# Kernel tuning notes

Hardware: AMD Instinct MI355X
Metric: run time of the kernel (lower is better)

## Reference

```python
import jax, jax.numpy as jnp
import numpy as np

N = 100000
IN_C = 256
OUT_C = 128
NHEAD = 4
NUM_CLASSES = 1000


def setup_inputs() -> dict:
    key = jax.random.key(0)
    ks = jax.random.split(key, 6)
    context_h = jax.random.normal(ks[0], (N, IN_C), dtype=jnp.float32)
    W_lin = jax.random.normal(ks[1], (NHEAD * OUT_C, IN_C), dtype=jnp.float32) * 0.05
    b_lin = jax.random.normal(ks[2], (NHEAD * OUT_C,), dtype=jnp.float32) * 0.05
    W_att = jax.random.normal(ks[3], (OUT_C,), dtype=jnp.float32) * 0.05
    b_att = jax.random.normal(ks[4], (1,), dtype=jnp.float32) * 0.05
    context_y = jax.random.randint(ks[5], (N,), 0, NUM_CLASSES, dtype=jnp.int32)
    return {
        "context_h": context_h,
        "W_lin": W_lin,
        "b_lin": b_lin,
        "W_att": W_att,
        "b_att": b_att,
        "context_y": context_y,
        "num_classes": NUM_CLASSES,
    }


def reference(context_h, W_lin, b_lin, W_att, b_att, context_y, num_classes):
    # Linear projection: [N, nhead*out_c] -> [N, nhead, out_c]
    h = context_h @ W_lin.T + b_lin
    n = context_h.shape[0]
    ht = h.reshape(n, NHEAD, OUT_C)
    # per-head attention score: [N, nhead]
    score = jnp.einsum("nho,o->nh", ht, W_att) + b_att[0]
    score = jnp.where(score >= 0, score, 0.2 * score)  # leaky_relu(0.2)
    # scatter softmax over segments context_y (stable two-pass)
    seg_max = jax.ops.segment_max(score, context_y, num_segments=num_classes)
    p = jnp.exp(score - seg_max[context_y])  # [N, nhead]
    denom = jax.ops.segment_sum(p, context_y, num_segments=num_classes)
    att_w = p / denom[context_y]  # [N, nhead]
    # weighted scatter-add pooling: [N, nhead, in_c] -> [C, nhead, in_c]
    att_h = context_h[:, None, :] * att_w[:, :, None]
    pooled = jax.ops.segment_sum(att_h, context_y, num_segments=num_classes)
    return pooled.reshape(num_classes, NHEAD * IN_C)
```

## Files before the change

### kernel.cpp

```cpp
#include <hip/hip_runtime.h>
#include <math.h>

#define N_ROWS 100000
#define IN_C   256
#define OUT_C  128
#define NHEAD  4
#define NCLS   1000
#define NCOPY  16
#define CAP    64

#define OFF_V      0
#define OFF_CB     1024
#define OFF_CNT    1032
#define OFF_BUCKET 17032

__global__ __launch_bounds__(256) void k_prep(const float* __restrict__ W_lin,
                                              const float* __restrict__ b_lin,
                                              const float* __restrict__ W_att,
                                              const float* __restrict__ b_att,
                                              float* __restrict__ ws) {
    const int b = blockIdx.x, t = threadIdx.x;
    if (b >= NHEAD) {
        int i = (b - NHEAD) * 256 + t;
        if (i < NCOPY * NCLS) ((unsigned*)(ws + OFF_CNT))[i] = 0u;
        return;
    }
    __shared__ float sw[OUT_C];
    __shared__ float rb[256];
    if (t < OUT_C) sw[t] = W_att[t];
    __syncthreads();
    const float* wl = W_lin + (size_t)(b * OUT_C) * IN_C + t;
    float s0 = 0.f, s1 = 0.f, s2 = 0.f, s3 = 0.f;
    #pragma unroll 8
    for (int o = 0; o < OUT_C; o += 4) {
        s0 = fmaf(wl[(size_t)(o + 0) * IN_C], sw[o + 0], s0);
        s1 = fmaf(wl[(size_t)(o + 1) * IN_C], sw[o + 1], s1);
        s2 = fmaf(wl[(size_t)(o + 2) * IN_C], sw[o + 2], s2);
        s3 = fmaf(wl[(size_t)(o + 3) * IN_C], sw[o + 3], s3);
    }
    (ws + OFF_V)[b * IN_C + t] = (s0 + s1) + (s2 + s3);
    rb[t] = (t < OUT_C) ? b_lin[b * OUT_C + t] * sw[t] : 0.f;
    __syncthreads();
    for (int d = 128; d; d >>= 1) {
        if (t < d) rb[t] += rb[t + d];
        __syncthreads();
    }
    if (t == 0) (ws + OFF_CB)[b] = rb[0] + b_att[0];
}

__global__ __launch_bounds__(256) void k_bucket(const int* __restrict__ y,
                                                float* __restrict__ ws) {
    int n = blockIdx.x * 256 + threadIdx.x;
    if (n >= N_ROWS) return;
    unsigned* cnt    = (unsigned*)(ws + OFF_CNT);
    unsigned* bucket = (unsigned*)(ws + OFF_BUCKET);
    unsigned idx = (blockIdx.x & (NCOPY - 1)) * NCLS + (unsigned)y[n];
    unsigned pos = atomicAdd(&cnt[idx], 1u);
    if (pos < CAP) bucket[idx * CAP + pos] = (unsigned)n;
}

__global__ __launch_bounds__(512) void k_pool(const float* __restrict__ ch,
                                              float* __restrict__ out,
                                              const float* __restrict__ ws) {
    __shared__ unsigned rowbuf[NCOPY * CAP];
    __shared__ float4   sAcc[NHEAD][4][64];
    __shared__ float4   sDs[8];
    const int c = blockIdx.x, t = threadIdx.x;
    const int wave = t >> 6, lane = t & 63;
    const unsigned* cntA   = (const unsigned*)(ws + OFF_CNT);
    const unsigned* bucket = (const unsigned*)(ws + OFF_BUCKET);
    float* o = out + (size_t)c * (NHEAD * IN_C);

    unsigned cc[NCOPY], pre[NCOPY];
    unsigned cnt = 0;
    #pragma unroll
    for (int cp = 0; cp < NCOPY; ++cp) {
        unsigned v = cntA[cp * NCLS + c];
        cc[cp] = v > CAP ? CAP : v;
        pre[cp] = cnt;
        cnt += cc[cp];
    }
    if (cnt == 0) {
        if (t < 256) ((float4*)o)[t] = make_float4(0.f, 0.f, 0.f, 0.f);
        return;
    }
    for (int tt = t; tt < NCOPY * CAP; tt += 512) {
        int cp = tt >> 6, j = tt & (CAP - 1);
        if ((unsigned)j < cc[cp])
            rowbuf[pre[cp] + j] = bucket[(cp * NCLS + c) * CAP + j];
    }
    __syncthreads();

    const float4* V4 = (const float4*)(ws + OFF_V);
    float4 v0 = V4[0 * 64 + lane];
    float4 v1 = V4[1 * 64 + lane];
    float4 v2 = V4[2 * 64 + lane];
    float4 v3 = V4[3 * 64 + lane];
    float4 cbv = *(const float4*)(ws + OFF_CB);
    float cb = (lane & 1) ? ((lane & 2) ? cbv.w : cbv.y)
                          : ((lane & 2) ? cbv.z : cbv.x);

    const float4* ch4 = (const float4*)ch;
    const float4 z = make_float4(0.f, 0.f, 0.f, 0.f);

    float4 a0 = z, a1 = z, a2 = z, a3 = z, dsum = z;
    {
        unsigned r = 2 * (unsigned)wave;
        float4 xA0 = z, xA1 = z, xB0 = z, xB1 = z;
        if (r < cnt)      xA0 = ch4[(size_t)rowbuf[r] * 64 + lane];
        if (r + 1 < cnt)  xA1 = ch4[(size_t)rowbuf[r + 1] * 64 + lane];
        if (r + 16 < cnt) xB0 = ch4[(size_t)rowbuf[r + 16] * 64 + lane];
        if (r + 17 < cnt) xB1 = ch4[(size_t)rowbuf[r + 17] * 64 + lane];
        for (; r < cnt; r += 16) {
            unsigned rc = r + 32;
            float4 xC0 = z, xC1 = z;
            if (rc < cnt)     xC0 = ch4[(size_t)rowbuf[rc] * 64 + lane];
            if (rc + 1 < cnt) xC1 = ch4[(size_t)rowbuf[rc + 1] * 64 + lane];

            #pragma unroll
            for (int k = 0; k < 2; ++k) {
                const float4 x = k ? xA1 : xA0;
                const float g = k ? ((r + 1 < cnt) ? 1.f : 0.f) : 1.f;
                float p0 = x.x * v0.x + x.y * v0.y + x.z * v0.z + x.w * v0.w;
                float p1 = x.x * v1.x + x.y * v1.y + x.z * v1.z + x.w * v1.w;
                float p2 = x.x * v2.x + x.y * v2.y + x.z * v2.z + x.w * v2.w;
                float p3 = x.x * v3.x + x.y * v3.y + x.z * v3.z + x.w * v3.w;
                float a01 = (lane & 1) ? p1 : p0;
                float b01 = (lane & 1) ? p0 : p1;
                b01 = __shfl_xor(b01, 1);  a01 += b01;
                float a23 = (lane & 1) ? p3 : p2;
                float b23 = (lane & 1) ? p2 : p3;
                b23 = __shfl_xor(b23, 1);  a23 += b23;
                float e = (lane & 2) ? a23 : a01;
                float f = (lane & 2) ? a01 : a23;
                f = __shfl_xor(f, 2);      e += f;
                e += __shfl_xor(e, 4);
                e += __shfl_xor(e, 8);
                e += __shfl_xor(e, 16);
                e += __shfl_xor(e, 32);
                float s = e + cb;
                s = s >= 0.0f ? s : 0.2f * s;
                float pe = expf(s) * g;
                float h0 = __shfl(pe, 0), h1 = __shfl(pe, 1);
                float h2 = __shfl(pe, 2), h3 = __shfl(pe, 3);
                dsum.x += h0; dsum.y += h1; dsum.z += h2; dsum.w += h3;
                a0.x = fmaf(x.x, h0, a0.x); a0.y = fmaf(x.y, h0, a0.y);
                a0.z = fmaf(x.z, h0, a0.z); a0.w = fmaf(x.w, h0, a0.w);
                a1.x = fmaf(x.x, h1, a1.x); a1.y = fmaf(x.y, h1, a1.y);
                a1.z = fmaf(x.z, h1, a1.z); a1.w = fmaf(x.w, h1, a1.w);
                a2.x = fmaf(x.x, h2, a2.x); a2.y = fmaf(x.y, h2, a2.y);
                a2.z = fmaf(x.z, h2, a2.z); a2.w = fmaf(x.w, h2, a2.w);
                a3.x = fmaf(x.x, h3, a3.x); a3.y = fmaf(x.y, h3, a3.y);
                a3.z = fmaf(x.z, h3, a3.z); a3.w = fmaf(x.w, h3, a3.w);
            }
            xA0 = xB0; xA1 = xB1; xB0 = xC0; xB1 = xC1;
        }
    }
    if (wave < 4) {
        sAcc[0][wave][lane] = a0; sAcc[1][wave][lane] = a1;
        sAcc[2][wave][lane] = a2; sAcc[3][wave][lane] = a3;
    }
    if (lane == 0) sDs[wave] = dsum;
    __syncthreads();
    if (wave >= 4) {
        int w = wave - 4;
        float4 q;
        q = sAcc[0][w][lane]; q.x += a0.x; q.y += a0.y; q.z += a0.z; q.w += a0.w; sAcc[0][w][lane] = q;
        q = sAcc[1][w][lane]; q.x += a1.x; q.y += a1.y; q.z += a1.z; q.w += a1.w; sAcc[1][w][lane] = q;
        q = sAcc[2][w][lane]; q.x += a2.x; q.y += a2.y; q.z += a2.z; q.w += a2.w; sAcc[2][w][lane] = q;
        q = sAcc[3][w][lane]; q.x += a3.x; q.y += a3.y; q.z += a3.z; q.w += a3.w; sAcc[3][w][lane] = q;
    }
    __syncthreads();

    if (wave < NHEAD) {
        float4 q0 = sAcc[wave][0][lane], q1 = sAcc[wave][1][lane],
               q2 = sAcc[wave][2][lane], q3 = sAcc[wave][3][lane];
        float4 acc = make_float4((q0.x + q1.x) + (q2.x + q3.x),
                                 (q0.y + q1.y) + (q2.y + q3.y),
                                 (q0.z + q1.z) + (q2.z + q3.z),
                                 (q0.w + q1.w) + (q2.w + q3.w));
        float4 d0 = sDs[0], d1 = sDs[1], d2 = sDs[2], d3 = sDs[3];
        float4 d4 = sDs[4], d5 = sDs[5], d6 = sDs[6], d7 = sDs[7];
        float4 dt = make_float4(((d0.x + d1.x) + (d2.x + d3.x)) + ((d4.x + d5.x) + (d6.x + d7.x)),
                                ((d0.y + d1.y) + (d2.y + d3.y)) + ((d4.y + d5.y) + (d6.y + d7.y)),
                                ((d0.z + d1.z) + (d2.z + d3.z)) + ((d4.z + d5.z) + (d6.z + d7.z)),
                                ((d0.w + d1.w) + (d2.w + d3.w)) + ((d4.w + d5.w) + (d6.w + d7.w)));
        float dh = (wave == 0) ? dt.x : (wave == 1) ? dt.y : (wave == 2) ? dt.z : dt.w;
        float inv = 1.0f / dh;
        ((float4*)o)[wave * 64 + lane] =
            make_float4(acc.x * inv, acc.y * inv, acc.z * inv, acc.w * inv);
    }
}

extern "C" void kernel_launch(void* const* d_in, const int* in_sizes, int n_in,
                              void* d_out, int out_size, void* d_ws, size_t ws_size,
                              hipStream_t stream) {
    const float* ch    = (const float*)d_in[0];
    const float* W_lin = (const float*)d_in[1];
    const float* b_lin = (const float*)d_in[2];
    const float* W_att = (const float*)d_in[3];
    const float* b_att = (const float*)d_in[4];
    const int*   y     = (const int*)d_in[5];
    float* out = (float*)d_out;
    float* ws  = (float*)d_ws;

    k_prep  <<<NHEAD + 63, 256, 0, stream>>>(W_lin, b_lin, W_att, b_att, ws);
    k_bucket<<<(N_ROWS + 255) / 256, 256, 0, stream>>>(y, ws);
    k_pool  <<<NCLS, 512, 0, stream>>>(ch, out, ws);
}
```

Before: 184.7 us.

## Split per-class pooling across four blocks and merge partials in a separate kernel

The pooling kernel used to run one 512-thread block per class, so only 1000 large blocks covered the GPU. It now launches four 256-thread blocks per class, each covering a quarter of the bucket copies and writing partial weighted sums and denominators to workspace. A new merge kernel adds the partials and normalises. This aims for better load balance and occupancy, at the cost of an extra launch and extra global traffic for the partials (about 16 MB written and then read back).

```diff
diff --git a/kernel.cpp b/kernel.cpp
--- a/kernel.cpp
+++ b/kernel.cpp
@@ -8,11 +8,15 @@
 #define NCLS   1000
 #define NCOPY  16
 #define CAP    64
+#define SPLIT  4
+#define CPS    (NCOPY / SPLIT)
 
 #define OFF_V      0
 #define OFF_CB     1024
 #define OFF_CNT    1032
 #define OFF_BUCKET 17032
+#define OFF_PART   1041032
+#define OFF_PDEN   5137032
 
 __global__ __launch_bounds__(256) void k_prep(const float* __restrict__ W_lin,
                                               const float* __restrict__ b_lin,
@@ -59,35 +63,38 @@
     if (pos < CAP) bucket[idx * CAP + pos] = (unsigned)n;
 }
 
-__global__ __launch_bounds__(512) void k_pool(const float* __restrict__ ch,
-                                              float* __restrict__ out,
-                                              const float* __restrict__ ws) {
-    __shared__ unsigned rowbuf[NCOPY * CAP];
-    __shared__ float4   sAcc[NHEAD][4][64];
-    __shared__ float4   sDs[8];
-    const int c = blockIdx.x, t = threadIdx.x;
-    const int wave = t >> 6, lane = t & 63;
+__global__ __launch_bounds__(256) void k_pool_part(const float* __restrict__ ch,
+                                                   float* __restrict__ ws) {
+    __shared__ unsigned rowbuf[CPS * CAP];
+    __shared__ float4   sAcc[NHEAD][2][64];
+    __shared__ float4   sDs[4];
+    const int c = blockIdx.x >> 2, seg = blockIdx.x & (SPLIT - 1);
+    const int t = threadIdx.x, wave = t >> 6, lane = t & 63;
     const unsigned* cntA   = (const unsigned*)(ws + OFF_CNT);
     const unsigned* bucket = (const unsigned*)(ws + OFF_BUCKET);
-    float* o = out + (size_t)c * (NHEAD * IN_C);
-
-    unsigned cc[NCOPY], pre[NCOPY];
+    float* part = ws + OFF_PART + (size_t)(seg * NCLS + c) * 1024;
+    float* pden = ws + OFF_PDEN + (seg * NCLS + c) * 4;
+    const float4 z = make_float4(0.f, 0.f, 0.f, 0.f);
+
+    unsigned cc[CPS], pre[CPS];
     unsigned cnt = 0;
     #pragma unroll
-    for (int cp = 0; cp < NCOPY; ++cp) {
-        unsigned v = cntA[cp * NCLS + c];
-        cc[cp] = v > CAP ? CAP : v;
-        pre[cp] = cnt;
-        cnt += cc[cp];
+    for (int j = 0; j < CPS; ++j) {
+        unsigned v = cntA[(seg * CPS + j) * NCLS + c];
+        cc[j] = v > CAP ? CAP : v;
+        pre[j] = cnt;
+        cnt += cc[j];
     }
     if (cnt == 0) {
-        if (t < 256) ((float4*)o)[t] = make_float4(0.f, 0.f, 0.f, 0.f);
+        ((float4*)part)[t] = z;
+        if (t < 4) pden[t] = 0.f;
         return;
     }
-    for (int tt = t; tt < NCOPY * CAP; tt += 512) {
-        int cp = tt >> 6, j = tt & (CAP - 1);
-        if ((unsigned)j < cc[cp])
-            rowbuf[pre[cp] + j] = bucket[(cp * NCLS + c) * CAP + j];
+    if (t < CAP) {
+        #pragma unroll
+        for (int j = 0; j < CPS; ++j)
+            if ((unsigned)t < cc[j])
+                rowbuf[pre[j] + t] = bucket[((seg * CPS + j) * NCLS + c) * CAP + t];
     }
     __syncthreads();
 
@@ -101,18 +108,17 @@
                           : ((lane & 2) ? cbv.z : cbv.x);
 
     const float4* ch4 = (const float4*)ch;
-    const float4 z = make_float4(0.f, 0.f, 0.f, 0.f);
 
     float4 a0 = z, a1 = z, a2 = z, a3 = z, dsum = z;
     {
         unsigned r = 2 * (unsigned)wave;
         float4 xA0 = z, xA1 = z, xB0 = z, xB1 = z;
-        if (r < cnt)      xA0 = ch4[(size_t)rowbuf[r] * 64 + lane];
-        if (r + 1 < cnt)  xA1 = ch4[(size_t)rowbuf[r + 1] * 64 + lane];
-        if (r + 16 < cnt) xB0 = ch4[(size_t)rowbuf[r + 16] * 64 + lane];
-        if (r + 17 < cnt) xB1 = ch4[(size_t)rowbuf[r + 17] * 64 + lane];
-        for (; r < cnt; r += 16) {
-            unsigned rc = r + 32;
+        if (r < cnt)     xA0 = ch4[(size_t)rowbuf[r] * 64 + lane];
+        if (r + 1 < cnt) xA1 = ch4[(size_t)rowbuf[r + 1] * 64 + lane];
+        if (r + 8 < cnt) xB0 = ch4[(size_t)rowbuf[r + 8] * 64 + lane];
+        if (r + 9 < cnt) xB1 = ch4[(size_t)rowbuf[r + 9] * 64 + lane];
+        for (; r < cnt; r += 8) {
+            unsigned rc = r + 16;
             float4 xC0 = z, xC1 = z;
             if (rc < cnt)     xC0 = ch4[(size_t)rowbuf[rc] * 64 + lane];
             if (rc + 1 < cnt) xC1 = ch4[(size_t)rowbuf[rc + 1] * 64 + lane];
@@ -156,14 +162,14 @@
             xA0 = xB0; xA1 = xB1; xB0 = xC0; xB1 = xC1;
         }
     }
-    if (wave < 4) {
+    if (wave < 2) {
         sAcc[0][wave][lane] = a0; sAcc[1][wave][lane] = a1;
         sAcc[2][wave][lane] = a2; sAcc[3][wave][lane] = a3;
     }
     if (lane == 0) sDs[wave] = dsum;
     __syncthreads();
-    if (wave >= 4) {
-        int w = wave - 4;
+    if (wave >= 2) {
+        int w = wave - 2;
         float4 q;
         q = sAcc[0][w][lane]; q.x += a0.x; q.y += a0.y; q.z += a0.z; q.w += a0.w; sAcc[0][w][lane] = q;
         q = sAcc[1][w][lane]; q.x += a1.x; q.y += a1.y; q.z += a1.z; q.w += a1.w; sAcc[1][w][lane] = q;
@@ -172,24 +178,39 @@
     }
     __syncthreads();
 
-    if (wave < NHEAD) {
-        float4 q0 = sAcc[wave][0][lane], q1 = sAcc[wave][1][lane],
-               q2 = sAcc[wave][2][lane], q3 = sAcc[wave][3][lane];
-        float4 acc = make_float4((q0.x + q1.x) + (q2.x + q3.x),
-                                 (q0.y + q1.y) + (q2.y + q3.y),
-                                 (q0.z + q1.z) + (q2.z + q3.z),
-                                 (q0.w + q1.w) + (q2.w + q3.w));
-        float4 d0 = sDs[0], d1 = sDs[1], d2 = sDs[2], d3 = sDs[3];
-        float4 d4 = sDs[4], d5 = sDs[5], d6 = sDs[6], d7 = sDs[7];
-        float4 dt = make_float4(((d0.x + d1.x) + (d2.x + d3.x)) + ((d4.x + d5.x) + (d6.x + d7.x)),
-                                ((d0.y + d1.y) + (d2.y + d3.y)) + ((d4.y + d5.y) + (d6.y + d7.y)),
-                                ((d0.z + d1.z) + (d2.z + d3.z)) + ((d4.z + d5.z) + (d6.z + d7.z)),
-                                ((d0.w + d1.w) + (d2.w + d3.w)) + ((d4.w + d5.w) + (d6.w + d7.w)));
-        float dh = (wave == 0) ? dt.x : (wave == 1) ? dt.y : (wave == 2) ? dt.z : dt.w;
-        float inv = 1.0f / dh;
-        ((float4*)o)[wave * 64 + lane] =
-            make_float4(acc.x * inv, acc.y * inv, acc.z * inv, acc.w * inv);
-    }
+    {
+        float4 q0 = sAcc[wave][0][lane], q1 = sAcc[wave][1][lane];
+        float4 acc = make_float4(q0.x + q1.x, q0.y + q1.y, q0.z + q1.z, q0.w + q1.w);
+        ((float4*)part)[wave * 64 + lane] = acc;
+        if (lane == 0) {
+            float4 d0 = sDs[0], d1 = sDs[1], d2 = sDs[2], d3 = sDs[3];
+            float4 dt = make_float4((d0.x + d1.x) + (d2.x + d3.x),
+                                    (d0.y + d1.y) + (d2.y + d3.y),
+                                    (d0.z + d1.z) + (d2.z + d3.z),
+                                    (d0.w + d1.w) + (d2.w + d3.w));
+            pden[wave] = (wave == 0) ? dt.x : (wave == 1) ? dt.y
+                       : (wave == 2) ? dt.z : dt.w;
+        }
+    }
+}
+
+__global__ __launch_bounds__(256) void k_merge(float* __restrict__ out,
+                                               const float* __restrict__ ws) {
+    const int c = blockIdx.x, t = threadIdx.x;
+    const float4* P = (const float4*)(ws + OFF_PART);
+    const float*  D = ws + OFF_PDEN;
+    const int head = t >> 6;
+    float4 a = make_float4(0.f, 0.f, 0.f, 0.f);
+    float den = 0.f;
+    #pragma unroll
+    for (int s = 0; s < SPLIT; ++s) {
+        float4 q = P[(size_t)(s * NCLS + c) * 256 + t];
+        a.x += q.x; a.y += q.y; a.z += q.z; a.w += q.w;
+        den += D[(s * NCLS + c) * 4 + head];
+    }
+    float inv = den > 0.f ? 1.0f / den : 0.f;
+    ((float4*)out)[(size_t)c * 256 + t] =
+        make_float4(a.x * inv, a.y * inv, a.z * inv, a.w * inv);
 }
 
 extern "C" void kernel_launch(void* const* d_in, const int* in_sizes, int n_in,
@@ -204,7 +225,8 @@
     float* out = (float*)d_out;
     float* ws  = (float*)d_ws;
 
-    k_prep  <<<NHEAD + 63, 256, 0, stream>>>(W_lin, b_lin, W_att, b_att, ws);
-    k_bucket<<<(N_ROWS + 255) / 256, 256, 0, stream>>>(y, ws);
-    k_pool  <<<NCLS, 512, 0, stream>>>(ch, out, ws);
-}
+    k_prep     <<<NHEAD + 63, 256, 0, stream>>>(W_lin, b_lin, W_att, b_att, ws);
+    k_bucket   <<<(N_ROWS + 255) / 256, 256, 0, stream>>>(y, ws);
+    k_pool_part<<<NCLS * SPLIT, 256, 0, stream>>>(ch, ws);
+    k_merge    <<<NCLS, 256, 0, stream>>>(out, ws);
+}
```

Measured after the change: 191.8 us. 1.04x slower.
